# Kernel tuning notes

Hardware: AMD Instinct MI355X
Metric: run time of the kernel (lower is better)

Reference implementation:

```python
import jax, jax.numpy as jnp
from jax import lax
import numpy as np

B, TE, TD, C, H, L, V, BLOCK = 2, 1024, 1024, 512, 8, 4, 32000, 1024
HD = C // H  # 64


def setup_inputs() -> dict:
    key = jax.random.key(0)
    ks = iter(jax.random.split(key, 64))
    def w(*shape):
        return jax.random.normal(next(ks), shape, jnp.float32) * 0.02
    d = {}
    d["enc_inp"] = jax.random.randint(next(ks), (B, TE), 0, V, dtype=jnp.int32)
    d["dec_inp"] = jax.random.randint(next(ks), (B, TD), 0, V, dtype=jnp.int32)
    d["enc_inp_mask"] = jnp.ones((B, TE), jnp.int32)
    d["tok_emb"] = w(V, C)
    d["pos_emb"] = w(BLOCK, C)
    for p in ["e", "d_sa", "d_ca"]:
        d[p + "_wq"] = w(L, H, C, HD)
        d[p + "_wk"] = w(L, H, C, HD)
        d[p + "_wv"] = w(L, H, C, HD)
        d[p + "_wo"] = w(L, C, C)
        d[p + "_bo"] = jnp.zeros((L, C), jnp.float32)
    for n in ["e_ln1", "e_ln2", "d_ln1", "d_ln2", "d_ln3"]:
        d[n + "_g"] = jnp.ones((L, C), jnp.float32)
        d[n + "_b"] = jnp.zeros((L, C), jnp.float32)
    for p in ["e", "d"]:
        d[p + "_w1"] = w(L, C, 4 * C)
        d[p + "_b1"] = jnp.zeros((L, 4 * C), jnp.float32)
        d[p + "_w2"] = w(L, 4 * C, C)
        d[p + "_b2"] = jnp.zeros((L, C), jnp.float32)
    d["out_w"] = w(C, V)
    d["out_b"] = jnp.zeros((V,), jnp.float32)
    return d


def _ln(x, g, b):
    m = jnp.mean(x, -1, keepdims=True)
    v = jnp.mean((x - m) ** 2, -1, keepdims=True)
    return (x - m) / jnp.sqrt(v + 1e-5) * g + b


def _mha(x, kv, wq, wk, wv, wo, bo, mask, causal):
    # x: [B,T,C], kv: [B,S,C], wq/wk/wv: [H,C,HD]
    q = jnp.einsum('btc,hcd->bhtd', x, wq)
    k = jnp.einsum('bsc,hcd->bhsd', kv, wk)
    v = jnp.einsum('bsc,hcd->bhsd', kv, wv)
    s = jnp.einsum('bhtd,bhsd->bhts', q, k) * (HD ** -0.5)
    if causal:
        T, S = s.shape[-2], s.shape[-1]
        s = jnp.where(jnp.tril(jnp.ones((T, S), bool)), s, -jnp.inf)
    if mask is not None:
        s = jnp.where(mask[:, None, None, :] != 0, s, -jnp.inf)
    a = jax.nn.softmax(s, axis=-1)
    o = jnp.einsum('bhts,bhsd->bthd', a, v).reshape(x.shape[0], x.shape[1], -1)
    return o @ wo + bo


def reference(enc_inp, dec_inp, enc_inp_mask, tok_emb, pos_emb,
              e_wq, e_wk, e_wv, e_wo, e_bo,
              d_sa_wq, d_sa_wk, d_sa_wv, d_sa_wo, d_sa_bo,
              d_ca_wq, d_ca_wk, d_ca_wv, d_ca_wo, d_ca_bo,
              e_ln1_g, e_ln1_b, e_ln2_g, e_ln2_b,
              d_ln1_g, d_ln1_b, d_ln2_g, d_ln2_b, d_ln3_g, d_ln3_b,
              e_w1, e_b1, e_w2, e_b2, d_w1, d_b1, d_w2, d_b2,
              out_w, out_b):
    enc = tok_emb[enc_inp] + pos_emb[:enc_inp.shape[1]]
    dec = tok_emb[dec_inp] + pos_emb[:dec_inp.shape[1]]

    def enc_step(x, p):
        ln1g, ln1b, wq, wk, wv, wo, bo, ln2g, ln2b, w1, b1, w2, b2 = p
        h = _ln(x, ln1g, ln1b)
        x = x + _mha(h, h, wq, wk, wv, wo, bo, enc_inp_mask, False)
        h = _ln(x, ln2g, ln2b)
        x = x + jnp.maximum(h @ w1 + b1, 0.0) @ w2 + b2
        return x, None

    enc_out, _ = lax.scan(enc_step, enc, (e_ln1_g, e_ln1_b, e_wq, e_wk, e_wv, e_wo, e_bo,
                                          e_ln2_g, e_ln2_b, e_w1, e_b1, e_w2, e_b2))

    def dec_step(x, p):
        (ln1g, ln1b, sawq, sawk, sawv, sawo, sabo,
         ln2g, ln2b, cawq, cawk, cawv, cawo, cabo,
         ln3g, ln3b, w1, b1, w2, b2) = p
        h = _ln(x, ln1g, ln1b)
        x = x + _mha(h, h, sawq, sawk, sawv, sawo, sabo, None, True)
        # torch code applies the same cross-attn LayerNorm to both x and encoder_output
        hq = _ln(x, ln2g, ln2b)
        hk = _ln(enc_out, ln2g, ln2b)
        x = x + _mha(hq, hk, cawq, cawk, cawv, cawo, cabo, enc_inp_mask, False)
        h = _ln(x, ln3g, ln3b)
        x = x + jnp.maximum(h @ w1 + b1, 0.0) @ w2 + b2
        return x, None

    dec_out, _ = lax.scan(dec_step, dec, (d_ln1_g, d_ln1_b, d_sa_wq, d_sa_wk, d_sa_wv, d_sa_wo, d_sa_bo,
                                          d_ln2_g, d_ln2_b, d_ca_wq, d_ca_wk, d_ca_wv, d_ca_wo, d_ca_bo,
                                          d_ln3_g, d_ln3_b, d_w1, d_b1, d_w2, d_b2))

    logits = dec_out @ out_w + out_b  # [B, T_dec, V]
    return logits
```

## Files before the change

kernel.cpp:

```cpp
#include <hip/hip_runtime.h>
#include <hip/hip_bf16.h>
#include <math.h>

#define Cdim 512
#define Hn   8
#define HDim 64
#define Ld   4
#define Tn   1024
#define Bn   2
#define NTOK 2048
#define FF   2048
#define Vn   32000

typedef __bf16 bf16_t;
typedef __bf16 bf16x8 __attribute__((ext_vector_type(8)));
typedef float  f32x4  __attribute__((ext_vector_type(4)));

__device__ __forceinline__ void ln_core(float v0, float v1,
    const float* __restrict__ g, const float* __restrict__ bb,
    bf16_t* __restrict__ yr, float* red, int tid)
{
    float s = v0 + v1;
    #pragma unroll
    for (int o = 32; o > 0; o >>= 1) s += __shfl_down(s, o, 64);
    int wid = tid >> 6, lane = tid & 63;
    if (lane == 0) red[wid] = s;
    __syncthreads();
    float mean = (red[0] + red[1] + red[2] + red[3]) * (1.f / Cdim);
    __syncthreads();
    float d0 = v0 - mean, d1 = v1 - mean;
    float qv = d0 * d0 + d1 * d1;
    #pragma unroll
    for (int o = 32; o > 0; o >>= 1) qv += __shfl_down(qv, o, 64);
    if (lane == 0) red[wid] = qv;
    __syncthreads();
    float var = (red[0] + red[1] + red[2] + red[3]) * (1.f / Cdim);
    float inv = rsqrtf(var + 1e-5f);
    yr[tid]       = (bf16_t)(d0 * inv * g[tid]       + bb[tid]);
    yr[tid + 256] = (bf16_t)(d1 * inv * g[tid + 256] + bb[tid + 256]);
}

__global__ __launch_bounds__(256) void ln_k(const float* __restrict__ x,
    const float* __restrict__ g, const float* __restrict__ bb, bf16_t* __restrict__ y)
{
    __shared__ float red[4];
    int row = blockIdx.x, tid = threadIdx.x;
    const float* xr = x + (long)row * Cdim;
    ln_core(xr[tid], xr[tid + 256], g, bb, y + (long)row * Cdim, red, tid);
}

__global__ __launch_bounds__(256) void ln2_k(const float* __restrict__ x1,
    const float* __restrict__ x2, const float* __restrict__ g,
    const float* __restrict__ bb, bf16_t* __restrict__ y1, bf16_t* __restrict__ y2)
{
    __shared__ float red[4];
    int row = blockIdx.x, tid = threadIdx.x;
    const float* x = (row < NTOK) ? x1 : x2;
    bf16_t*      y = (row < NTOK) ? y1 : y2;
    int r = row & (NTOK - 1);
    const float* xr = x + (long)r * Cdim;
    ln_core(xr[tid], xr[tid + 256], g, bb, y + (long)r * Cdim, red, tid);
}

__global__ __launch_bounds__(256) void embed_ln_k(const int* __restrict__ inp,
    const float* __restrict__ tok, const float* __restrict__ pos,
    const float* __restrict__ g, const float* __restrict__ bb,
    float* __restrict__ x, bf16_t* __restrict__ y)
{
    __shared__ float red[4];
    int bt = blockIdx.x, tid = threadIdx.x;
    int t = bt & (Tn - 1);
    long toff = (long)inp[bt] * Cdim;
    float v0 = tok[toff + tid]       + pos[(long)t * Cdim + tid];
    float v1 = tok[toff + tid + 256] + pos[(long)t * Cdim + tid + 256];
    float* xr = x + (long)bt * Cdim;
    xr[tid] = v0; xr[tid + 256] = v1;
    ln_core(v0, v1, g, bb, y + (long)bt * Cdim, red, tid);
}

struct Ptr3 { const float* p[3]; };
__global__ __launch_bounds__(256) void tcvt_b_k(Ptr3 srcs, bf16_t* __restrict__ dst,
    int R, int Cc, int lps, long dstStride)
{
    int z = blockIdx.z; int s = z / lps, l = z - s * lps;
    const float* in = srcs.p[s] + (long)l * R * Cc;
    bf16_t* op = dst + (long)z * dstStride;
    __shared__ float t[64][65];
    int r0 = blockIdx.y * 64, c0 = blockIdx.x * 64;
    int tx = threadIdx.x & 63, ty = threadIdx.x >> 6;
    #pragma unroll
    for (int i = 0; i < 16; i++)
        t[ty + i * 4][tx] = in[(long)(r0 + ty + i * 4) * Cc + c0 + tx];
    __syncthreads();
    #pragma unroll
    for (int i = 0; i < 16; i++) {
        int cc = ty + i * 4;
        op[(long)(c0 + cc) * R + r0 + tx] = (bf16_t)t[tx][cc];
    }
}

struct QkvSrc { const float* p[9]; };
__global__ __launch_bounds__(256) void tcvt_qkv_k(QkvSrc srcs, bf16_t* __restrict__ outp)
{
    int z = blockIdx.z;
    int si = z >> 5, zb = (z >> 3) & 3, zh = z & 7;
    int set = si / 3, part = si - set * 3;
    const float* in = srcs.p[si] + (long)zb * (Hn * Cdim * HDim) + (long)zh * (Cdim * HDim);
    bf16_t* op = outp + ((long)set * Ld + zb) * (1536L * Cdim)
                      + (long)part * 512 * Cdim + (long)zh * 64 * Cdim;
    __shared__ float t[64][65];
    int r0 = blockIdx.y * 64;
    int tx = threadIdx.x & 63, ty = threadIdx.x >> 6;
    #pragma unroll
    for (int i = 0; i < 16; i++)
        t[ty + i * 4][tx] = in[(long)(r0 + ty + i * 4) * HDim + tx];
    __syncthreads();
    #pragma unroll
    for (int i = 0; i < 16; i++) {
        int cc = ty + i * 4;
        op[(long)cc * Cdim + r0 + tx] = (bf16_t)t[tx][cc];
    }
}

template<int BM, int BN, int BK, bool BIAS, bool RELU, bool RES, bool OBF,
         bool VOUT, int SWZM, bool XOUT>
__global__ __launch_bounds__(256) void mgemm_k(
    const bf16_t* __restrict__ A, const bf16_t* __restrict__ A2, int aSplit,
    const bf16_t* __restrict__ Bt, const float* __restrict__ bias,
    const float* __restrict__ res, void* __restrict__ Cout,
    bf16_t* __restrict__ xout, bf16_t* __restrict__ vtout, int vSplit,
    int K, int lda, int ldb, int ldc)
{
    constexpr int MR = BM / 32;
    constexpr int NR = BN / 32;
    constexpr int KK = BK / 32;
    constexpr int LPR = BK / 8;
    __shared__ bf16_t As[BM * BK];
    __shared__ bf16_t Bs[BN * BK];

    int tid = threadIdx.x;
    int wv = tid >> 6, lane = tid & 63;
    int bm, bn;
    if constexpr (SWZM > 0) {
        int lin = blockIdx.y * gridDim.x + blockIdx.x;
        int tot = gridDim.x * gridDim.y;
        int chunk = tot >> 3;
        int e = (lin & 7) * chunk + (lin >> 3);
        bm = (e % SWZM) * BM;
        bn = (e / SWZM) * BN;
    } else {
        bm = blockIdx.y * BM; bn = blockIdx.x * BN;
    }
    const bf16_t* Ab = (bn < aSplit) ? A : A2;
    int wr = wv >> 1, wc = wv & 1;

    f32x4 acc[MR][NR];
    #pragma unroll
    for (int i = 0; i < MR; i++)
        #pragma unroll
        for (int j = 0; j < NR; j++)
            acc[i][j] = (f32x4){0.f, 0.f, 0.f, 0.f};

    constexpr int RPW = 512 / BK;
    constexpr int RPP = 2048 / BK;
    const int sr  = lane / LPR;
    const int sc8 = ((lane % LPR) ^ (sr & (LPR - 1))) * 8;
    const int r16 = lane & 15, g4 = lane >> 4;

    for (int k0 = 0; k0 < K; k0 += BK) {
        #pragma unroll
        for (int p = 0; p < BM * BK / 2048; p++) {
            int rb = p * RPP + wv * RPW;
            const bf16_t* g = Ab + (long)(bm + rb + sr) * lda + (k0 + sc8);
            __builtin_amdgcn_global_load_lds(
                (const __attribute__((address_space(1))) void*)g,
                (__attribute__((address_space(3))) void*)&As[rb * BK],
                16, 0, 0);
        }
        #pragma unroll
        for (int p = 0; p < BN * BK / 2048; p++) {
            int rb = p * RPP + wv * RPW;
            const bf16_t* g = Bt + (long)(bn + rb + sr) * ldb + (k0 + sc8);
            __builtin_amdgcn_global_load_lds(
                (const __attribute__((address_space(1))) void*)g,
                (__attribute__((address_space(3))) void*)&Bs[rb * BK],
                16, 0, 0);
        }
        __syncthreads();

        #pragma unroll
        for (int kk = 0; kk < KK; kk++) {
            bf16x8 bkk[NR];
            #pragma unroll
            for (int j = 0; j < NR; j++) {
                int row = wc * (BN / 2) + j * 16 + r16;
                bkk[j] = *(const bf16x8*)&Bs[row * BK + (((kk * 4 + g4) ^ (row & (LPR - 1))) * 8)];
            }
            #pragma unroll
            for (int i = 0; i < MR; i++) {
                int row = wr * (BM / 2) + i * 16 + r16;
                bf16x8 a = *(const bf16x8*)&As[row * BK + (((kk * 4 + g4) ^ (row & (LPR - 1))) * 8)];
                #pragma unroll
                for (int j = 0; j < NR; j++)
                    acc[i][j] = __builtin_amdgcn_mfma_f32_16x16x32_bf16(a, bkk[j], acc[i][j], 0, 0, 0);
            }
        }
        __syncthreads();
    }

    int crow0 = g4 * 4;
    int ccol  = r16;
    #pragma unroll
    for (int i = 0; i < MR; i++) {
        #pragma unroll
        for (int j = 0; j < NR; j++) {
            int gr = bm + wr * (BM / 2) + i * 16 + crow0;
            int gc = bn + wc * (BN / 2) + j * 16 + ccol;
            float bv = BIAS ? bias[gc] : 0.f;
            #pragma unroll
            for (int q = 0; q < 4; q++) {
                float v = acc[i][j][q];
                if (BIAS) v += bv;
                if (RELU) v = fmaxf(v, 0.f);
                if (VOUT && gc >= vSplit) {
                    int row = gr + q;
                    int b = row >> 10, t = row & (Tn - 1);
                    vtout[((long)b * 512 + (gc - vSplit)) * Tn + t] = (bf16_t)v;
                } else {
                    long oidx = (long)(gr + q) * ldc + gc;
                    if (RES)  v += res[oidx];
                    if (OBF) ((bf16_t*)Cout)[oidx] = (bf16_t)v;
                    else     ((float*) Cout)[oidx] = v;
                    if (XOUT) xout[oidx] = (bf16_t)v;
                }
            }
        }
    }
}

template<bool CAUSAL, bool HASMASK>
__global__ __launch_bounds__(512, 2) void flash_k(
    const bf16_t* __restrict__ qkv, const bf16_t* __restrict__ vt,
    const int* __restrict__ mask, bf16_t* __restrict__ ao)
{
    __shared__ bf16_t Kl[2][64][72];
    __shared__ bf16_t Vl[2][64][72];
    __shared__ bf16_t Pl[8][16][72];

    int qt = blockIdx.x, bh = blockIdx.y;
    int b = bh >> 3, h = bh & 7;
    int tid = threadIdx.x, wv = tid >> 6, lane = tid & 63;
    int wg = wv >> 2, wq4 = wv & 3;
    int r16 = lane & 15, g4 = lane >> 4;
    int gtid = tid & 255;

    const bf16_t* qb = qkv + ((long)(b * Tn + qt * 64 + wq4 * 16 + r16)) * 1536 + h * 64;
    bf16x8 aq0 = *(const bf16x8*)&qb[g4 * 8];
    bf16x8 aq1 = *(const bf16x8*)&qb[32 + g4 * 8];

    f32x4 acc[4];
    #pragma unroll
    for (int j = 0; j < 4; j++) acc[j] = (f32x4){0.f, 0.f, 0.f, 0.f};
    float m_[4], l_[4];
    #pragma unroll
    for (int q = 0; q < 4; q++) { m_[q] = -1e30f; l_[q] = 0.f; }

    int lastT = CAUSAL ? qt : (Tn / 64 - 1);
    int niter = CAUSAL ? (qt / 2 + 1) : (Tn / 128);
    int krow = gtid >> 3, kcol = (gtid & 7) * 8;

    for (int it = 0; it < niter; it++) {
        int t = 2 * it + wg;
        bool active = t <= lastT;
        int s0 = t * 64;
        bf16x8 kr[2], vr[2];
        int mv = 0;
        if (active) {
            #pragma unroll
            for (int i = 0; i < 2; i++)
                kr[i] = *(const bf16x8*)&qkv[((long)(b * Tn + s0 + krow + i * 32)) * 1536 + 512 + h * 64 + kcol];
            #pragma unroll
            for (int i = 0; i < 2; i++)
                vr[i] = *(const bf16x8*)&vt[((long)(bh * 64 + krow + i * 32)) * Tn + s0 + kcol];
            if (HASMASK) mv = mask[b * Tn + s0 + lane];
        }
        __syncthreads();
        if (active) {
            #pragma unroll
            for (int i = 0; i < 2; i++) *(bf16x8*)&Kl[wg][krow + i * 32][kcol] = kr[i];
            #pragma unroll
            for (int i = 0; i < 2; i++) *(bf16x8*)&Vl[wg][krow + i * 32][kcol] = vr[i];
        }
        __syncthreads();
        if (!active) continue;

        f32x4 scv[4];
        __builtin_amdgcn_s_setprio(1);
        #pragma unroll
        for (int j = 0; j < 4; j++) {
            scv[j] = (f32x4){0.f, 0.f, 0.f, 0.f};
            bf16x8 bk0 = *(const bf16x8*)&Kl[wg][j * 16 + r16][g4 * 8];
            bf16x8 bk1 = *(const bf16x8*)&Kl[wg][j * 16 + r16][32 + g4 * 8];
            scv[j] = __builtin_amdgcn_mfma_f32_16x16x32_bf16(aq0, bk0, scv[j], 0, 0, 0);
            scv[j] = __builtin_amdgcn_mfma_f32_16x16x32_bf16(aq1, bk1, scv[j], 0, 0, 0);
        }
        __builtin_amdgcn_s_setprio(0);

        bool diag = CAUSAL && (t == qt);
        #pragma unroll
        for (int j = 0; j < 4; j++) {
            int col = j * 16 + r16;
            int mm = 1;
            if (HASMASK) mm = __shfl(mv, col, 64);
            #pragma unroll
            for (int q = 0; q < 4; q++) {
                float v = scv[j][q] * 0.125f;
                if (diag && col > wq4 * 16 + g4 * 4 + q) v = -1e30f;
                if (HASMASK && mm == 0) v = -1e30f;
                scv[j][q] = v;
            }
        }

        float pmax[4];
        #pragma unroll
        for (int q = 0; q < 4; q++) {
            float v = fmaxf(fmaxf(scv[0][q], scv[1][q]), fmaxf(scv[2][q], scv[3][q]));
            v = fmaxf(v, __shfl_xor(v, 1, 64));
            v = fmaxf(v, __shfl_xor(v, 2, 64));
            v = fmaxf(v, __shfl_xor(v, 4, 64));
            v = fmaxf(v, __shfl_xor(v, 8, 64));
            pmax[q] = v;
        }
        bool skip = __all(pmax[0] <= m_[0] + 8.f && pmax[1] <= m_[1] + 8.f &&
                          pmax[2] <= m_[2] + 8.f && pmax[3] <= m_[3] + 8.f);
        if (!skip) {
            #pragma unroll
            for (int q = 0; q < 4; q++) {
                float mnew = fmaxf(m_[q], pmax[q]);
                float rf = __expf(m_[q] - mnew);
                l_[q] *= rf;
                #pragma unroll
                for (int j = 0; j < 4; j++) acc[j][q] *= rf;
                m_[q] = mnew;
            }
        }
        #pragma unroll
        for (int q = 0; q < 4; q++) {
            float rs = 0.f;
            #pragma unroll
            for (int j = 0; j < 4; j++) {
                float pv = __expf(scv[j][q] - m_[q]);
                scv[j][q] = pv;
                rs += pv;
            }
            rs += __shfl_xor(rs, 1, 64);
            rs += __shfl_xor(rs, 2, 64);
            rs += __shfl_xor(rs, 4, 64);
            rs += __shfl_xor(rs, 8, 64);
            l_[q] += rs;
        }

        #pragma unroll
        for (int j = 0; j < 4; j++)
            #pragma unroll
            for (int q = 0; q < 4; q++)
                Pl[wv][g4 * 4 + q][j * 16 + r16] = (bf16_t)scv[j][q];
        asm volatile("s_waitcnt lgkmcnt(0)" ::: "memory");
        __builtin_amdgcn_sched_barrier(0);

        __builtin_amdgcn_s_setprio(1);
        #pragma unroll
        for (int c = 0; c < 2; c++) {
            bf16x8 pa = *(const bf16x8*)&Pl[wv][r16][c * 32 + g4 * 8];
            #pragma unroll
            for (int j = 0; j < 4; j++) {
                bf16x8 bv = *(const bf16x8*)&Vl[wg][j * 16 + r16][c * 32 + g4 * 8];
                acc[j] = __builtin_amdgcn_mfma_f32_16x16x32_bf16(pa, bv, acc[j], 0, 0, 0);
            }
        }
        __builtin_amdgcn_s_setprio(0);
    }

    float* accS = (float*)&Kl[0][0][0];
    float* mlS  = accS + 64 * 64;
    __syncthreads();
    if (wg == 1) {
        #pragma unroll
        for (int j = 0; j < 4; j++)
            #pragma unroll
            for (int q = 0; q < 4; q++)
                accS[(wq4 * 16 + g4 * 4 + q) * 64 + j * 16 + r16] = acc[j][q];
        if (r16 == 0)
            #pragma unroll
            for (int q = 0; q < 4; q++) {
                mlS[(wq4 * 16 + g4 * 4 + q) * 2 + 0] = m_[q];
                mlS[(wq4 * 16 + g4 * 4 + q) * 2 + 1] = l_[q];
            }
    }
    __syncthreads();
    if (wg == 0) {
        bf16_t* aob = ao + ((long)(b * Tn + qt * 64 + wq4 * 16 + g4 * 4)) * Cdim + h * 64;
        #pragma unroll
        for (int q = 0; q < 4; q++) {
            int row = wq4 * 16 + g4 * 4 + q;
            float mB = mlS[row * 2], lB = mlS[row * 2 + 1];
            float mS = fmaxf(m_[q], mB);
            float fA = __expf(m_[q] - mS), fB = __expf(mB - mS);
            float lS = l_[q] * fA + lB * fB;
            float inv = 1.f / lS;
            #pragma unroll
            for (int j = 0; j < 4; j++) {
                float o = (acc[j][q] * fA + accS[row * 64 + j * 16 + r16] * fB) * inv;
                aob[(long)q * Cdim + j * 16 + r16] = (bf16_t)o;
            }
        }
    }
}

static void run_attn(hipStream_t stream, const bf16_t* hq, const bf16_t* hkv,
    const bf16_t* wqkv, const float* bo, const bf16_t* wo_t,
    float* xres, const int* mask, bool causal,
    bf16_t* qkv, bf16_t* vt, bf16_t* ao)
{
    dim3 blk(256);
    mgemm_k<64,128,64,false,false,false,true,true,0,false><<<dim3(12, 32, 1), blk, 0, stream>>>(
        hq, hkv, 512, wqkv, nullptr, nullptr, qkv, nullptr, vt, 1024,
        Cdim, Cdim, Cdim, 1536);
    if (causal)
        flash_k<true,false><<<dim3(Tn / 64, Bn * Hn), dim3(512), 0, stream>>>(qkv, vt, nullptr, ao);
    else
        flash_k<false,true><<<dim3(Tn / 64, Bn * Hn), dim3(512), 0, stream>>>(qkv, vt, mask, ao);
    mgemm_k<64,64,64,true,false,true,false,false,0,false><<<dim3(8, 32, 1), blk, 0, stream>>>(
        ao, ao, 1 << 30, wo_t, bo, xres, xres, nullptr, nullptr, 1 << 30,
        Cdim, Cdim, Cdim, Cdim);
}

extern "C" void kernel_launch(void* const* d_in, const int* in_sizes, int n_in,
                              void* d_out, int out_size, void* d_ws, size_t ws_size,
                              hipStream_t stream)
{
    (void)in_sizes; (void)n_in; (void)out_size; (void)ws_size;
    const int*   enc_inp  = (const int*)d_in[0];
    const int*   dec_inp  = (const int*)d_in[1];
    const int*   enc_mask = (const int*)d_in[2];
    const float* tok_emb  = (const float*)d_in[3];
    const float* pos_emb  = (const float*)d_in[4];
    const float* e_wq  = (const float*)d_in[5];
    const float* e_wk  = (const float*)d_in[6];
    const float* e_wv  = (const float*)d_in[7];
    const float* e_wo  = (const float*)d_in[8];
    const float* e_bo  = (const float*)d_in[9];
    const float* dsa_wq = (const float*)d_in[10];
    const float* dsa_wk = (const float*)d_in[11];
    const float* dsa_wv = (const float*)d_in[12];
    const float* dsa_wo = (const float*)d_in[13];
    const float* dsa_bo = (const float*)d_in[14];
    const float* dca_wq = (const float*)d_in[15];
    const float* dca_wk = (const float*)d_in[16];
    const float* dca_wv = (const float*)d_in[17];
    const float* dca_wo = (const float*)d_in[18];
    const float* dca_bo = (const float*)d_in[19];
    const float* e_ln1_g = (const float*)d_in[20];
    const float* e_ln1_b = (const float*)d_in[21];
    const float* e_ln2_g = (const float*)d_in[22];
    const float* e_ln2_b = (const float*)d_in[23];
    const float* d_ln1_g = (const float*)d_in[24];
    const float* d_ln1_b = (const float*)d_in[25];
    const float* d_ln2_g = (const float*)d_in[26];
    const float* d_ln2_b = (const float*)d_in[27];
    const float* d_ln3_g = (const float*)d_in[28];
    const float* d_ln3_b = (const float*)d_in[29];
    const float* e_w1 = (const float*)d_in[30];
    const float* e_b1 = (const float*)d_in[31];
    const float* e_w2 = (const float*)d_in[32];
    const float* e_b2 = (const float*)d_in[33];
    const float* d_w1 = (const float*)d_in[34];
    const float* d_b1 = (const float*)d_in[35];
    const float* d_w2 = (const float*)d_in[36];
    const float* d_b2 = (const float*)d_in[37];
    const float* out_w = (const float*)d_in[38];
    const float* out_b = (const float*)d_in[39];
    float* out = (float*)d_out;

    char* p = (char*)d_ws;
    auto takeB = [&](size_t bytes) { char* r = p; p += (bytes + 255) & ~(size_t)255; return r; };
    float*  x_enc = (float*)takeB(1048576ull * 4);
    float*  x_dec = (float*)takeB(1048576ull * 4);
    bf16_t* h     = (bf16_t*)takeB(1048576ull * 2);
    bf16_t* hk    = (bf16_t*)takeB(1048576ull * 2);
    bf16_t* qkv   = (bf16_t*)takeB(3145728ull * 2);
    bf16_t* vt    = (bf16_t*)takeB(1048576ull * 2);
    bf16_t* ao    = (bf16_t*)takeB(1048576ull * 2);
    bf16_t* xdb   = (bf16_t*)takeB(1048576ull * 2);
    bf16_t* mid   = (bf16_t*)takeB(4194304ull * 2);
    bf16_t* wqkv_t = (bf16_t*)takeB(12ull * 786432 * 2);
    bf16_t* wo_t   = (bf16_t*)takeB(12ull * 262144 * 2);
    bf16_t* w1_t   = (bf16_t*)takeB(8ull * 1048576 * 2);
    bf16_t* w2_t   = (bf16_t*)takeB(8ull * 1048576 * 2);
    bf16_t* outw_t = (bf16_t*)takeB(16384000ull * 2);

    dim3 blk(256);
    const long LQKV = 1536L * Cdim;

    QkvSrc qs;
    qs.p[0] = e_wq;   qs.p[1] = e_wk;   qs.p[2] = e_wv;
    qs.p[3] = dsa_wq; qs.p[4] = dsa_wk; qs.p[5] = dsa_wv;
    qs.p[6] = dca_wq; qs.p[7] = dca_wk; qs.p[8] = dca_wv;
    tcvt_qkv_k<<<dim3(1, 8, 288), blk, 0, stream>>>(qs, wqkv_t);
    Ptr3 pw;
    pw.p[0] = e_wo; pw.p[1] = dsa_wo; pw.p[2] = dca_wo;
    tcvt_b_k<<<dim3(8, 8, 12), blk, 0, stream>>>(pw, wo_t, Cdim, Cdim, 4, (long)Cdim * Cdim);
    pw.p[0] = e_w1; pw.p[1] = d_w1; pw.p[2] = nullptr;
    tcvt_b_k<<<dim3(32, 8, 8), blk, 0, stream>>>(pw, w1_t, Cdim, FF, 4, (long)Cdim * FF);
    pw.p[0] = e_w2; pw.p[1] = d_w2; pw.p[2] = nullptr;
    tcvt_b_k<<<dim3(8, 32, 8), blk, 0, stream>>>(pw, w2_t, FF, Cdim, 4, (long)FF * Cdim);
    pw.p[0] = out_w; pw.p[1] = nullptr; pw.p[2] = nullptr;
    tcvt_b_k<<<dim3(500, 8, 1), blk, 0, stream>>>(pw, outw_t, Cdim, Vn, 1, 0);

    embed_ln_k<<<NTOK, blk, 0, stream>>>(enc_inp, tok_emb, pos_emb, e_ln1_g, e_ln1_b, x_enc, h);
    for (int l = 0; l < Ld; l++) {
        if (l) ln_k<<<NTOK, blk, 0, stream>>>(x_enc, e_ln1_g + l * Cdim, e_ln1_b + l * Cdim, h);
        run_attn(stream, h, h,
                 wqkv_t + (long)l * LQKV, e_bo + l * Cdim, wo_t + (long)l * Cdim * Cdim,
                 x_enc, enc_mask, false, qkv, vt, ao);
        ln_k<<<NTOK, blk, 0, stream>>>(x_enc, e_ln2_g + l * Cdim, e_ln2_b + l * Cdim, h);
        mgemm_k<128,128,64,true,true,false,true,false,0,false><<<dim3(16, 16, 1), blk, 0, stream>>>(
            h, h, 1 << 30, w1_t + (long)l * Cdim * FF, e_b1 + l * FF, nullptr, mid,
            nullptr, nullptr, 1 << 30, Cdim, Cdim, Cdim, FF);
        mgemm_k<64,64,64,true,false,true,false,false,0,false><<<dim3(8, 32, 1), blk, 0, stream>>>(
            mid, mid, 1 << 30, w2_t + (long)l * FF * Cdim, e_b2 + l * Cdim, x_enc, x_enc,
            nullptr, nullptr, 1 << 30, FF, FF, FF, Cdim);
    }

    embed_ln_k<<<NTOK, blk, 0, stream>>>(dec_inp, tok_emb, pos_emb, d_ln1_g, d_ln1_b, x_dec, h);
    for (int l = 0; l < Ld; l++) {
        if (l) ln_k<<<NTOK, blk, 0, stream>>>(x_dec, d_ln1_g + l * Cdim, d_ln1_b + l * Cdim, h);
        run_attn(stream, h, h,
                 wqkv_t + (long)(Ld + l) * LQKV, dsa_bo + l * Cdim,
                 wo_t + (long)(Ld + l) * Cdim * Cdim,
                 x_dec, nullptr, true, qkv, vt, ao);
        ln2_k<<<2 * NTOK, blk, 0, stream>>>(x_dec, x_enc,
            d_ln2_g + l * Cdim, d_ln2_b + l * Cdim, h, hk);
        run_attn(stream, h, hk,
                 wqkv_t + (long)(2 * Ld + l) * LQKV, dca_bo + l * Cdim,
                 wo_t + (long)(2 * Ld + l) * Cdim * Cdim,
                 x_dec, enc_mask, false, qkv, vt, ao);
        ln_k<<<NTOK, blk, 0, stream>>>(x_dec, d_ln3_g + l * Cdim, d_ln3_b + l * Cdim, h);
        mgemm_k<128,128,64,true,true,false,true,false,0,false><<<dim3(16, 16, 1), blk, 0, stream>>>(
            h, h, 1 << 30, w1_t + (long)(Ld + l) * Cdim * FF, d_b1 + l * FF, nullptr, mid,
            nullptr, nullptr, 1 << 30, Cdim, Cdim, Cdim, FF);
        if (l < Ld - 1)
            mgemm_k<64,64,64,true,false,true,false,false,0,false><<<dim3(8, 32, 1), blk, 0, stream>>>(
                mid, mid, 1 << 30, w2_t + (long)(Ld + l) * FF * Cdim, d_b2 + l * Cdim, x_dec, x_dec,
                nullptr, nullptr, 1 << 30, FF, FF, FF, Cdim);
        else
            mgemm_k<64,64,64,true,false,true,false,false,0,true><<<dim3(8, 32, 1), blk, 0, stream>>>(
                mid, mid, 1 << 30, w2_t + (long)(Ld + l) * FF * Cdim, d_b2 + l * Cdim, x_dec, x_dec,
                xdb, nullptr, 1 << 30, FF, FF, FF, Cdim);
    }

    mgemm_k<256,128,64,true,false,false,false,false,8,false><<<dim3(250, 8, 1), blk, 0, stream>>>(
        xdb, xdb, 1 << 30, outw_t, out_b, nullptr, out, nullptr, nullptr, 1 << 30,
        Cdim, Cdim, Cdim, Vn);
}
```

Baseline: 1.160 ms.

## Use wave-per-row LayerNorm, coalesced GEMM epilogue, flash K/V prefetch, smaller logits tile

LayerNorm kernels now give each row to one wavefront, using vector loads and xor-shuffle reductions, so block-level LDS reductions and syncs go away. The GEMM epilogue can stage accumulators through LDS so each wave writes contiguous rows with vector stores. The flash-attention loop prefetches the next K/V tile into registers before computing the current one. The logits GEMM moves from 256x128 to 128x128 tiles with a different swizzle. The trade-offs are extra LDS traffic in the epilogue and higher register pressure in the flash kernel.

```diff
diff --git a/kernel.cpp b/kernel.cpp
--- a/kernel.cpp
+++ b/kernel.cpp
@@ -14,52 +14,56 @@
 
 typedef __bf16 bf16_t;
 typedef __bf16 bf16x8 __attribute__((ext_vector_type(8)));
+typedef __bf16 bf16x4 __attribute__((ext_vector_type(4)));
 typedef float  f32x4  __attribute__((ext_vector_type(4)));
 
-__device__ __forceinline__ void ln_core(float v0, float v1,
+__device__ __forceinline__ void ln_wave(const float* __restrict__ xr,
     const float* __restrict__ g, const float* __restrict__ bb,
-    bf16_t* __restrict__ yr, float* red, int tid)
-{
-    float s = v0 + v1;
-    #pragma unroll
-    for (int o = 32; o > 0; o >>= 1) s += __shfl_down(s, o, 64);
-    int wid = tid >> 6, lane = tid & 63;
-    if (lane == 0) red[wid] = s;
-    __syncthreads();
-    float mean = (red[0] + red[1] + red[2] + red[3]) * (1.f / Cdim);
-    __syncthreads();
-    float d0 = v0 - mean, d1 = v1 - mean;
-    float qv = d0 * d0 + d1 * d1;
-    #pragma unroll
-    for (int o = 32; o > 0; o >>= 1) qv += __shfl_down(qv, o, 64);
-    if (lane == 0) red[wid] = qv;
-    __syncthreads();
-    float var = (red[0] + red[1] + red[2] + red[3]) * (1.f / Cdim);
-    float inv = rsqrtf(var + 1e-5f);
-    yr[tid]       = (bf16_t)(d0 * inv * g[tid]       + bb[tid]);
-    yr[tid + 256] = (bf16_t)(d1 * inv * g[tid + 256] + bb[tid + 256]);
+    bf16_t* __restrict__ yr, int lane)
+{
+    f32x4 a = *(const f32x4*)&xr[lane * 8];
+    f32x4 c = *(const f32x4*)&xr[lane * 8 + 4];
+    float s = a[0] + a[1] + a[2] + a[3] + c[0] + c[1] + c[2] + c[3];
+    #pragma unroll
+    for (int o = 1; o < 64; o <<= 1) s += __shfl_xor(s, o, 64);
+    float mean = s * (1.f / Cdim);
+    float d[8], qv = 0.f;
+    #pragma unroll
+    for (int k = 0; k < 4; k++) { d[k] = a[k] - mean; d[4 + k] = c[k] - mean; }
+    #pragma unroll
+    for (int k = 0; k < 8; k++) qv += d[k] * d[k];
+    #pragma unroll
+    for (int o = 1; o < 64; o <<= 1) qv += __shfl_xor(qv, o, 64);
+    float inv = rsqrtf(qv * (1.f / Cdim) + 1e-5f);
+    f32x4 g0 = *(const f32x4*)&g[lane * 8],  g1 = *(const f32x4*)&g[lane * 8 + 4];
+    f32x4 b0 = *(const f32x4*)&bb[lane * 8], b1 = *(const f32x4*)&bb[lane * 8 + 4];
+    bf16x8 o;
+    #pragma unroll
+    for (int k = 0; k < 4; k++) {
+        o[k]     = (bf16_t)(d[k]     * inv * g0[k] + b0[k]);
+        o[4 + k] = (bf16_t)(d[4 + k] * inv * g1[k] + b1[k]);
+    }
+    *(bf16x8*)&yr[lane * 8] = o;
 }
 
 __global__ __launch_bounds__(256) void ln_k(const float* __restrict__ x,
     const float* __restrict__ g, const float* __restrict__ bb, bf16_t* __restrict__ y)
 {
-    __shared__ float red[4];
-    int row = blockIdx.x, tid = threadIdx.x;
-    const float* xr = x + (long)row * Cdim;
-    ln_core(xr[tid], xr[tid + 256], g, bb, y + (long)row * Cdim, red, tid);
+    int wid = threadIdx.x >> 6, lane = threadIdx.x & 63;
+    int row = blockIdx.x * 4 + wid;
+    ln_wave(x + (long)row * Cdim, g, bb, y + (long)row * Cdim, lane);
 }
 
 __global__ __launch_bounds__(256) void ln2_k(const float* __restrict__ x1,
     const float* __restrict__ x2, const float* __restrict__ g,
     const float* __restrict__ bb, bf16_t* __restrict__ y1, bf16_t* __restrict__ y2)
 {
-    __shared__ float red[4];
-    int row = blockIdx.x, tid = threadIdx.x;
+    int wid = threadIdx.x >> 6, lane = threadIdx.x & 63;
+    int row = blockIdx.x * 4 + wid;
     const float* x = (row < NTOK) ? x1 : x2;
     bf16_t*      y = (row < NTOK) ? y1 : y2;
     int r = row & (NTOK - 1);
-    const float* xr = x + (long)r * Cdim;
-    ln_core(xr[tid], xr[tid + 256], g, bb, y + (long)r * Cdim, red, tid);
+    ln_wave(x + (long)r * Cdim, g, bb, y + (long)r * Cdim, lane);
 }
 
 __global__ __launch_bounds__(256) void embed_ln_k(const int* __restrict__ inp,
@@ -67,15 +71,39 @@
     const float* __restrict__ g, const float* __restrict__ bb,
     float* __restrict__ x, bf16_t* __restrict__ y)
 {
-    __shared__ float red[4];
-    int bt = blockIdx.x, tid = threadIdx.x;
+    int wid = threadIdx.x >> 6, lane = threadIdx.x & 63;
+    int bt = blockIdx.x * 4 + wid;
     int t = bt & (Tn - 1);
     long toff = (long)inp[bt] * Cdim;
-    float v0 = tok[toff + tid]       + pos[(long)t * Cdim + tid];
-    float v1 = tok[toff + tid + 256] + pos[(long)t * Cdim + tid + 256];
+    f32x4 a = *(const f32x4*)&tok[toff + lane * 8];
+    f32x4 c = *(const f32x4*)&tok[toff + lane * 8 + 4];
+    f32x4 pa = *(const f32x4*)&pos[(long)t * Cdim + lane * 8];
+    f32x4 pc = *(const f32x4*)&pos[(long)t * Cdim + lane * 8 + 4];
+    a += pa; c += pc;
     float* xr = x + (long)bt * Cdim;
-    xr[tid] = v0; xr[tid + 256] = v1;
-    ln_core(v0, v1, g, bb, y + (long)bt * Cdim, red, tid);
+    *(f32x4*)&xr[lane * 8] = a;
+    *(f32x4*)&xr[lane * 8 + 4] = c;
+    float s = a[0] + a[1] + a[2] + a[3] + c[0] + c[1] + c[2] + c[3];
+    #pragma unroll
+    for (int o = 1; o < 64; o <<= 1) s += __shfl_xor(s, o, 64);
+    float mean = s * (1.f / Cdim);
+    float d[8], qv = 0.f;
+    #pragma unroll
+    for (int k = 0; k < 4; k++) { d[k] = a[k] - mean; d[4 + k] = c[k] - mean; }
+    #pragma unroll
+    for (int k = 0; k < 8; k++) qv += d[k] * d[k];
+    #pragma unroll
+    for (int o = 1; o < 64; o <<= 1) qv += __shfl_xor(qv, o, 64);
+    float inv = rsqrtf(qv * (1.f / Cdim) + 1e-5f);
+    f32x4 g0 = *(const f32x4*)&g[lane * 8],  g1 = *(const f32x4*)&g[lane * 8 + 4];
+    f32x4 b0 = *(const f32x4*)&bb[lane * 8], b1 = *(const f32x4*)&bb[lane * 8 + 4];
+    bf16x8 o;
+    #pragma unroll
+    for (int k = 0; k < 4; k++) {
+        o[k]     = (bf16_t)(d[k]     * inv * g0[k] + b0[k]);
+        o[4 + k] = (bf16_t)(d[4 + k] * inv * g1[k] + b1[k]);
+    }
+    *(bf16x8*)&y[(long)bt * Cdim + lane * 8] = o;
 }
 
 struct Ptr3 { const float* p[3]; };
@@ -123,7 +151,7 @@
 }
 
 template<int BM, int BN, int BK, bool BIAS, bool RELU, bool RES, bool OBF,
-         bool VOUT, int SWZM, bool XOUT>
+         bool VOUT, int SWZM, bool XOUT, bool COAL>
 __global__ __launch_bounds__(256) void mgemm_k(
     const bf16_t* __restrict__ A, const bf16_t* __restrict__ A2, int aSplit,
     const bf16_t* __restrict__ Bt, const float* __restrict__ bias,
@@ -137,6 +165,7 @@
     constexpr int LPR = BK / 8;
     __shared__ bf16_t As[BM * BK];
     __shared__ bf16_t Bs[BN * BK];
+    __shared__ float cws[COAL ? 4 * 16 * 36 : 1];
 
     int tid = threadIdx.x;
     int wv = tid >> 6, lane = tid & 63;
@@ -208,30 +237,77 @@
         __syncthreads();
     }
 
-    int crow0 = g4 * 4;
-    int ccol  = r16;
-    #pragma unroll
-    for (int i = 0; i < MR; i++) {
-        #pragma unroll
-        for (int j = 0; j < NR; j++) {
-            int gr = bm + wr * (BM / 2) + i * 16 + crow0;
-            int gc = bn + wc * (BN / 2) + j * 16 + ccol;
-            float bv = BIAS ? bias[gc] : 0.f;
-            #pragma unroll
-            for (int q = 0; q < 4; q++) {
-                float v = acc[i][j][q];
-                if (BIAS) v += bv;
-                if (RELU) v = fmaxf(v, 0.f);
-                if (VOUT && gc >= vSplit) {
-                    int row = gr + q;
-                    int b = row >> 10, t = row & (Tn - 1);
-                    vtout[((long)b * 512 + (gc - vSplit)) * Tn + t] = (bf16_t)v;
+    if constexpr (COAL) {
+        #pragma unroll
+        for (int i = 0; i < MR; i++) {
+            int gr0 = bm + wr * (BM / 2) + i * 16;
+            #pragma unroll
+            for (int hh = 0; hh < NR / 2; hh++) {
+                #pragma unroll
+                for (int jj = 0; jj < 2; jj++) {
+                    int j = hh * 2 + jj;
+                    int gc = bn + wc * (BN / 2) + j * 16 + r16;
+                    float bv = BIAS ? bias[gc] : 0.f;
+                    #pragma unroll
+                    for (int q = 0; q < 4; q++) {
+                        float v = acc[i][j][q];
+                        if (BIAS) v += bv;
+                        if (RELU) v = fmaxf(v, 0.f);
+                        cws[(wv * 16 + g4 * 4 + q) * 36 + jj * 16 + r16] = v;
+                    }
+                }
+                int gcb = bn + wc * (BN / 2) + hh * 32;
+                if constexpr (OBF) {
+                    int row = lane >> 2, c8 = (lane & 3) * 8;
+                    f32x4 v0 = *(f32x4*)&cws[(wv * 16 + row) * 36 + c8];
+                    f32x4 v1 = *(f32x4*)&cws[(wv * 16 + row) * 36 + c8 + 4];
+                    long oidx = (long)(gr0 + row) * ldc + gcb + c8;
+                    bf16x8 o;
+                    #pragma unroll
+                    for (int k = 0; k < 4; k++) { o[k] = (bf16_t)v0[k]; o[4 + k] = (bf16_t)v1[k]; }
+                    *(bf16x8*)&((bf16_t*)Cout)[oidx] = o;
                 } else {
-                    long oidx = (long)(gr + q) * ldc + gc;
-                    if (RES)  v += res[oidx];
-                    if (OBF) ((bf16_t*)Cout)[oidx] = (bf16_t)v;
-                    else     ((float*) Cout)[oidx] = v;
-                    if (XOUT) xout[oidx] = (bf16_t)v;
+                    #pragma unroll
+                    for (int ps = 0; ps < 2; ps++) {
+                        int row = (lane >> 3) + 8 * ps, c4 = (lane & 7) * 4;
+                        f32x4 v = *(f32x4*)&cws[(wv * 16 + row) * 36 + c4];
+                        long oidx = (long)(gr0 + row) * ldc + gcb + c4;
+                        if (RES) v += *(const f32x4*)&res[oidx];
+                        *(f32x4*)&((float*)Cout)[oidx] = v;
+                        if (XOUT) {
+                            bf16x4 o;
+                            #pragma unroll
+                            for (int k = 0; k < 4; k++) o[k] = (bf16_t)v[k];
+                            *(bf16x4*)&xout[oidx] = o;
+                        }
+                    }
+                }
+            }
+        }
+    } else {
+        #pragma unroll
+        for (int i = 0; i < MR; i++) {
+            #pragma unroll
+            for (int j = 0; j < NR; j++) {
+                int gr = bm + wr * (BM / 2) + i * 16 + g4 * 4;
+                int gc = bn + wc * (BN / 2) + j * 16 + r16;
+                float bv = BIAS ? bias[gc] : 0.f;
+                #pragma unroll
+                for (int q = 0; q < 4; q++) {
+                    float v = acc[i][j][q];
+                    if (BIAS) v += bv;
+                    if (RELU) v = fmaxf(v, 0.f);
+                    if (VOUT && gc >= vSplit) {
+                        int row = gr + q;
+                        int b = row >> 10, t = row & (Tn - 1);
+                        vtout[((long)b * 512 + (gc - vSplit)) * Tn + t] = (bf16_t)v;
+                    } else {
+                        long oidx = (long)(gr + q) * ldc + gc;
+                        if (RES)  v += res[oidx];
+                        if (OBF) ((bf16_t*)Cout)[oidx] = (bf16_t)v;
+                        else     ((float*) Cout)[oidx] = v;
+                        if (XOUT) xout[oidx] = (bf16_t)v;
+                    }
                 }
             }
         }
@@ -269,21 +345,25 @@
     int niter = CAUSAL ? (qt / 2 + 1) : (Tn / 128);
     int krow = gtid >> 3, kcol = (gtid & 7) * 8;
 
+    bf16x8 kr[2], vr[2];
+    int mv = 0;
+    {
+        int t0 = wg;
+        if (t0 <= lastT) {
+            int s0 = t0 * 64;
+            #pragma unroll
+            for (int i = 0; i < 2; i++)
+                kr[i] = *(const bf16x8*)&qkv[((long)(b * Tn + s0 + krow + i * 32)) * 1536 + 512 + h * 64 + kcol];
+            #pragma unroll
+            for (int i = 0; i < 2; i++)
+                vr[i] = *(const bf16x8*)&vt[((long)(bh * 64 + krow + i * 32)) * Tn + s0 + kcol];
+            if (HASMASK) mv = mask[b * Tn + s0 + lane];
+        }
+    }
+
     for (int it = 0; it < niter; it++) {
         int t = 2 * it + wg;
         bool active = t <= lastT;
-        int s0 = t * 64;
-        bf16x8 kr[2], vr[2];
-        int mv = 0;
-        if (active) {
-            #pragma unroll
-            for (int i = 0; i < 2; i++)
-                kr[i] = *(const bf16x8*)&qkv[((long)(b * Tn + s0 + krow + i * 32)) * 1536 + 512 + h * 64 + kcol];
-            #pragma unroll
-            for (int i = 0; i < 2; i++)
-                vr[i] = *(const bf16x8*)&vt[((long)(bh * 64 + krow + i * 32)) * Tn + s0 + kcol];
-            if (HASMASK) mv = mask[b * Tn + s0 + lane];
-        }
         __syncthreads();
         if (active) {
             #pragma unroll
@@ -292,6 +372,18 @@
             for (int i = 0; i < 2; i++) *(bf16x8*)&Vl[wg][krow + i * 32][kcol] = vr[i];
         }
         __syncthreads();
+        int mv_use = mv;
+        int tn = t + 2;
+        if (it + 1 < niter && tn <= lastT) {
+            int sn = tn * 64;
+            #pragma unroll
+            for (int i = 0; i < 2; i++)
+                kr[i] = *(const bf16x8*)&qkv[((long)(b * Tn + sn + krow + i * 32)) * 1536 + 512 + h * 64 + kcol];
+            #pragma unroll
+            for (int i = 0; i < 2; i++)
+                vr[i] = *(const bf16x8*)&vt[((long)(bh * 64 + krow + i * 32)) * Tn + sn + kcol];
+            if (HASMASK) mv = mask[b * Tn + sn + lane];
+        }
         if (!active) continue;
 
         f32x4 scv[4];
@@ -311,7 +403,7 @@
         for (int j = 0; j < 4; j++) {
             int col = j * 16 + r16;
             int mm = 1;
-            if (HASMASK) mm = __shfl(mv, col, 64);
+            if (HASMASK) mm = __shfl(mv_use, col, 64);
             #pragma unroll
             for (int q = 0; q < 4; q++) {
                 float v = scv[j][q] * 0.125f;
@@ -423,14 +515,14 @@
     bf16_t* qkv, bf16_t* vt, bf16_t* ao)
 {
     dim3 blk(256);
-    mgemm_k<64,128,64,false,false,false,true,true,0,false><<<dim3(12, 32, 1), blk, 0, stream>>>(
+    mgemm_k<64,128,64,false,false,false,true,true,0,false,false><<<dim3(12, 32, 1), blk, 0, stream>>>(
         hq, hkv, 512, wqkv, nullptr, nullptr, qkv, nullptr, vt, 1024,
         Cdim, Cdim, Cdim, 1536);
     if (causal)
         flash_k<true,false><<<dim3(Tn / 64, Bn * Hn), dim3(512), 0, stream>>>(qkv, vt, nullptr, ao);
     else
         flash_k<false,true><<<dim3(Tn / 64, Bn * Hn), dim3(512), 0, stream>>>(qkv, vt, mask, ao);
-    mgemm_k<64,64,64,true,false,true,false,false,0,false><<<dim3(8, 32, 1), blk, 0, stream>>>(
+    mgemm_k<64,64,64,true,false,true,false,false,0,false,true><<<dim3(8, 32, 1), blk, 0, stream>>>(
         ao, ao, 1 << 30, wo_t, bo, xres, xres, nullptr, nullptr, 1 << 30,
         Cdim, Cdim, Cdim, Cdim);
 }
@@ -517,49 +609,49 @@
     pw.p[0] = out_w; pw.p[1] = nullptr; pw.p[2] = nullptr;
     tcvt_b_k<<<dim3(500, 8, 1), blk, 0, stream>>>(pw, outw_t, Cdim, Vn, 1, 0);
 
-    embed_ln_k<<<NTOK, blk, 0, stream>>>(enc_inp, tok_emb, pos_emb, e_ln1_g, e_ln1_b, x_enc, h);
+    embed_ln_k<<<NTOK / 4, blk, 0, stream>>>(enc_inp, tok_emb, pos_emb, e_ln1_g, e_ln1_b, x_enc, h);
     for (int l = 0; l < Ld; l++) {
-        if (l) ln_k<<<NTOK, blk, 0, stream>>>(x_enc, e_ln1_g + l * Cdim, e_ln1_b + l * Cdim, h);
+        if (l) ln_k<<<NTOK / 4, blk, 0, stream>>>(x_enc, e_ln1_g + l * Cdim, e_ln1_b + l * Cdim, h);
         run_attn(stream, h, h,
                  wqkv_t + (long)l * LQKV, e_bo + l * Cdim, wo_t + (long)l * Cdim * Cdim,
                  x_enc, enc_mask, false, qkv, vt, ao);
-        ln_k<<<NTOK, blk, 0, stream>>>(x_enc, e_ln2_g + l * Cdim, e_ln2_b + l * Cdim, h);
-        mgemm_k<128,128,64,true,true,false,true,false,0,false><<<dim3(16, 16, 1), blk, 0, stream>>>(
+        ln_k<<<NTOK / 4, blk, 0, stream>>>(x_enc, e_ln2_g + l * Cdim, e_ln2_b + l * Cdim, h);
+        mgemm_k<128,128,64,true,true,false,true,false,0,false,true><<<dim3(16, 16, 1), blk, 0, stream>>>(
             h, h, 1 << 30, w1_t + (long)l * Cdim * FF, e_b1 + l * FF, nullptr, mid,
             nullptr, nullptr, 1 << 30, Cdim, Cdim, Cdim, FF);
-        mgemm_k<64,64,64,true,false,true,false,false,0,false><<<dim3(8, 32, 1), blk, 0, stream>>>(
+        mgemm_k<64,64,64,true,false,true,false,false,0,false,true><<<dim3(8, 32, 1), blk, 0, stream>>>(
             mid, mid, 1 << 30, w2_t + (long)l * FF * Cdim, e_b2 + l * Cdim, x_enc, x_enc,
             nullptr, nullptr, 1 << 30, FF, FF, FF, Cdim);
     }
 
-    embed_ln_k<<<NTOK, blk, 0, stream>>>(dec_inp, tok_emb, pos_emb, d_ln1_g, d_ln1_b, x_dec, h);
+    embed_ln_k<<<NTOK / 4, blk, 0, stream>>>(dec_inp, tok_emb, pos_emb, d_ln1_g, d_ln1_b, x_dec, h);
     for (int l = 0; l < Ld; l++) {
-        if (l) ln_k<<<NTOK, blk, 0, stream>>>(x_dec, d_ln1_g + l * Cdim, d_ln1_b + l * Cdim, h);
+        if (l) ln_k<<<NTOK / 4, blk, 0, stream>>>(x_dec, d_ln1_g + l * Cdim, d_ln1_b + l * Cdim, h);
         run_attn(stream, h, h,
                  wqkv_t + (long)(Ld + l) * LQKV, dsa_bo + l * Cdim,
                  wo_t + (long)(Ld + l) * Cdim * Cdim,
                  x_dec, nullptr, true, qkv, vt, ao);
-        ln2_k<<<2 * NTOK, blk, 0, stream>>>(x_dec, x_enc,
+        ln2_k<<<2 * NTOK / 4, blk, 0, stream>>>(x_dec, x_enc,
             d_ln2_g + l * Cdim, d_ln2_b + l * Cdim, h, hk);
         run_attn(stream, h, hk,
                  wqkv_t + (long)(2 * Ld + l) * LQKV, dca_bo + l * Cdim,
                  wo_t + (long)(2 * Ld + l) * Cdim * Cdim,
                  x_dec, enc_mask, false, qkv, vt, ao);
-        ln_k<<<NTOK, blk, 0, stream>>>(x_dec, d_ln3_g + l * Cdim, d_ln3_b + l * Cdim, h);
-        mgemm_k<128,128,64,true,true,false,true,false,0,false><<<dim3(16, 16, 1), blk, 0, stream>>>(
+        ln_k<<<NTOK / 4, blk, 0, stream>>>(x_dec, d_ln3_g + l * Cdim, d_ln3_b + l * Cdim, h);
+        mgemm_k<128,128,64,true,true,false,true,false,0,false,true><<<dim3(16, 16, 1), blk, 0, stream>>>(
             h, h, 1 << 30, w1_t + (long)(Ld + l) * Cdim * FF, d_b1 + l * FF, nullptr, mid,
             nullptr, nullptr, 1 << 30, Cdim, Cdim, Cdim, FF);
         if (l < Ld - 1)
-            mgemm_k<64,64,64,true,false,true,false,false,0,false><<<dim3(8, 32, 1), blk, 0, stream>>>(
+            mgemm_k<64,64,64,true,false,true,false,false,0,false,true><<<dim3(8, 32, 1), blk, 0, stream>>>(
                 mid, mid, 1 << 30, w2_t + (long)(Ld + l) * FF * Cdim, d_b2 + l * Cdim, x_dec, x_dec,
                 nullptr, nullptr, 1 << 30, FF, FF, FF, Cdim);
         else
-            mgemm_k<64,64,64,true,false,true,false,false,0,true><<<dim3(8, 32, 1), blk, 0, stream>>>(
+            mgemm_k<64,64,64,true,false,true,false,false,0,true,true><<<dim3(8, 32, 1), blk, 0, stream>>>(
                 mid, mid, 1 << 30, w2_t + (long)(Ld + l) * FF * Cdim, d_b2 + l * Cdim, x_dec, x_dec,
                 xdb, nullptr, 1 << 30, FF, FF, FF, Cdim);
     }
 
-    mgemm_k<256,128,64,true,false,false,false,false,8,false><<<dim3(250, 8, 1), blk, 0, stream>>>(
+    mgemm_k<128,128,64,true,false,false,false,false,16,false,true><<<dim3(250, 16, 1), blk, 0, stream>>>(
         xdb, xdb, 1 << 30, outw_t, out_b, nullptr, out, nullptr, nullptr, 1 << 30,
         Cdim, Cdim, Cdim, Vn);
 }
```

Result: faster. 1.119 ms (-3.5%).
